# Kernel tuning notes

Measured on AMD Instinct MI355X. Metric: run time of the kernel, lower is better.

Reference implementation:

```python
import jax, jax.numpy as jnp
import numpy as np

SELECT_SIZE = 64
SM_SCALE = 0.07216878364870322  # 192 ** -0.5
V_HEAD_DIM = 128


def setup_inputs() -> dict:
    key = jax.random.key(0)
    k1, k2, k3, k4 = jax.random.split(key, 4)
    B, S, Hq, G, TOPK = 4, 2048, 16, 4, 16
    T = B * S
    NB = S // SELECT_SIZE  # 32 blocks per sequence
    q = jax.random.normal(k1, (T, Hq, 192), dtype=jnp.float32)
    k = jax.random.normal(k2, (T, Hq, 192), dtype=jnp.float32)
    v = jax.random.normal(k3, (T, Hq, V_HEAD_DIM), dtype=jnp.float32)
    idx = jax.random.randint(k4, (T, G, TOPK), 0, NB, dtype=jnp.int32)
    # guarantee block 0 is always selected so every causal row has >=1 valid key
    idx = idx.at[..., 0].set(0)
    idx = jnp.sort(idx, axis=-1)
    return {"q": q, "k": k, "v": v, "selected_indices": idx,
            "batch_size": B, "seq_len": S}


def reference(q, k, v, selected_indices, batch_size, seq_len):
    B, S = batch_size, seq_len
    Hq = q.shape[1]
    G = selected_indices.shape[1]
    Hg = Hq // G  # query heads per selection-score group
    nb = (S + SELECT_SIZE - 1) // SELECT_SIZE
    dv = v.shape[-1]

    # un-ragged: B equal-length sequences
    qg = q.reshape(B, S, G, Hg, -1)
    kg = k.reshape(B, S, G, Hg, -1)
    vg = v.reshape(B, S, G, Hg, -1)
    idx = selected_indices.reshape(B, S, G, -1)

    # which KV blocks are selected for each (query position, group): [B,S,G,nb]
    allowed_blk = (idx[..., None] == jnp.arange(nb, dtype=idx.dtype)).any(axis=-2)
    blk_of_pos = jnp.arange(S) // SELECT_SIZE
    pos_ok = allowed_blk[..., blk_of_pos]  # [B, Tq, G, Skv]
    causal = jnp.arange(S)[:, None] >= jnp.arange(S)[None, :]
    mask = pos_ok & causal[None, :, None, :]          # [B, Tq, G, Skv]
    mask = mask.transpose(0, 2, 1, 3)[:, :, None]      # [B, G, 1, Tq, Skv]

    scores = jnp.einsum('btghd,bsghd->bghts', qg, kg) * SM_SCALE
    scores = jnp.where(mask, scores, jnp.float32(-1e30))
    attn = jax.nn.softmax(scores, axis=-1)
    o = jnp.einsum('bghts,bsghd->btghd', attn, vg)
    return o.reshape(B * S, Hq * dv)
```

## Files before the change

kernel.cpp:

```cpp
#include <hip/hip_runtime.h>


typedef __attribute__((ext_vector_type(8))) _Float16 half8;
typedef __attribute__((ext_vector_type(4))) float f32x4;
typedef __attribute__((ext_vector_type(4))) unsigned int u32x4;

__device__ __forceinline__ half8 cvt8(const float4* p) {
  float4 a = p[0], b = p[1];
  half8 r;
  r[0] = (_Float16)a.x; r[1] = (_Float16)a.y; r[2] = (_Float16)a.z; r[3] = (_Float16)a.w;
  r[4] = (_Float16)b.x; r[5] = (_Float16)b.y; r[6] = (_Float16)b.z; r[7] = (_Float16)b.w;
  return r;
}

__device__ __forceinline__ half8 cvt8s(const float4* p, float s) {
  float4 a = p[0], b = p[1];
  half8 r;
  r[0] = (_Float16)(a.x * s); r[1] = (_Float16)(a.y * s);
  r[2] = (_Float16)(a.z * s); r[3] = (_Float16)(a.w * s);
  r[4] = (_Float16)(b.x * s); r[5] = (_Float16)(b.y * s);
  r[6] = (_Float16)(b.z * s); r[7] = (_Float16)(b.w * s);
  return r;
}

__device__ __forceinline__ void async16(const void* g, void* l) {
  __builtin_amdgcn_global_load_lds(
      (const __attribute__((address_space(1))) void*)g,
      (__attribute__((address_space(3))) void*)l, 16, 0, 0);
}

__device__ __forceinline__ f32x4 vmax4(f32x4 a, f32x4 b) {
  f32x4 r;
  r[0] = fmaxf(a[0], b[0]); r[1] = fmaxf(a[1], b[1]);
  r[2] = fmaxf(a[2], b[2]); r[3] = fmaxf(a[3], b[3]);
  return r;
}

__global__ __launch_bounds__(256) void kv_prep(const float* __restrict__ k,
                                               const float* __restrict__ v,
                                               _Float16* __restrict__ kf,
                                               _Float16* __restrict__ vf) {
  __shared__ float lb[64 * 196];
  int blk = blockIdx.x;
  int bh = blk >> 5, kb = blk & 31;
  int b = bh >> 4, h = bh & 15;
  int tid = threadIdx.x;

  const float* ksrc = k + ((long)(b * 2048 + kb * 64) * 16 + h) * 192;
#pragma unroll
  for (int it = 0; it < 12; ++it) {
    int idx = it * 256 + tid;
    int kk = idx / 48, c4 = idx - kk * 48;
    *(float4*)(&lb[kk * 196 + c4 * 4]) = *(const float4*)(ksrc + (long)kk * 3072 + c4 * 4);
  }
  __syncthreads();
  _Float16* kdst = kf + (long)blk * 12288;
#pragma unroll
  for (int it = 0; it < 6; ++it) {
    int oct = it * 256 + tid;
    int frag = oct >> 6, lane = oct & 63;
    int ntile = frag / 6, kc = frag - ntile * 6;
    int lm = lane & 15;
    int n = ((lm >> 2) << 4) + ntile * 4 + (lm & 3);
    int d = kc * 32 + ((lane >> 4) << 3);
    *(half8*)(kdst + (long)oct * 8) = cvt8((const float4*)(&lb[n * 196 + d]));
  }
  __syncthreads();

  const float* vsrc = v + ((long)(b * 2048 + kb * 64) * 16 + h) * 128;
#pragma unroll
  for (int it = 0; it < 8; ++it) {
    int idx = it * 256 + tid;
    int kk = idx >> 5, c4 = idx & 31;
    *(float4*)(&lb[kk * 132 + c4 * 4]) = *(const float4*)(vsrc + (long)kk * 2048 + c4 * 4);
  }
  __syncthreads();
  _Float16* vdst = vf + (long)blk * 8192;
#pragma unroll
  for (int it = 0; it < 4; ++it) {
    int oct = it * 256 + tid;
    int frag = oct >> 6, lane = oct & 63;
    int n0 = frag >> 1, kc = frag & 1;
    int dv = n0 * 16 + (lane & 15);
    int kbase = kc * 32 + ((lane >> 4) << 3);
    half8 o;
#pragma unroll
    for (int j = 0; j < 8; ++j) o[j] = (_Float16)lb[(kbase + j) * 132 + dv];
    *(half8*)(vdst + (long)oct * 8) = o;
  }
}

__global__ __launch_bounds__(256) void attn_main(const float* __restrict__ q,
                                                 const int* __restrict__ idx,
                                                 const _Float16* __restrict__ kf,
                                                 const _Float16* __restrict__ vf,
                                                 float* __restrict__ out) {
  constexpr float SCL = 0.07216878364870322f * 1.4426950408889634f;
  int id = (int)blockIdx.x;
  int qb = 31 - (id >> 6);
  int h = id & 15, b = (id >> 4) & 3, g = h >> 2;
  int tid = threadIdx.x;
  int w = tid >> 6, L = tid & 63;
  int Lm = L & 15, Lq = L >> 4;
  int m0 = w * 16;
  int t0 = b * 2048 + qb * 64;

  __shared__ __align__(16) char sh_k[24576];

  const char* kfb = (const char*)(kf + (long)((b * 16 + h) * 32) * 12288);
  const _Float16* vfb = vf + (long)((b * 16 + h) * 32) * 8192;

  auto stageK = [&](int kb) {
#pragma unroll
    for (int c = 0; c < 6; ++c) {
      int ch = w + c * 4;
      async16(kfb + (long)kb * 24576 + ch * 1024 + L * 16, sh_k + ch * 1024);
    }
  };

  half8 vr[16];
  auto loadV = [&](int kb) {
    const half8* vg = (const half8*)(vfb + (long)kb * 8192);
#pragma unroll
    for (int j = 0; j < 16; ++j) vr[j] = vg[j * 64 + L];
  };

  half8 qa[6];
  const float* qrow = q + ((long)(t0 + m0 + Lm) * 16 + h) * 192;
#pragma unroll
  for (int c = 0; c < 6; ++c) qa[c] = cvt8s((const float4*)(qrow + c * 32 + Lq * 8), SCL);

  unsigned rm = 0;
  {
    const int4* ip = (const int4*)(idx + ((long)(t0 + L) * 4 + g) * 16);
#pragma unroll
    for (int u = 0; u < 4; ++u) {
      int4 iv = ip[u];
      rm |= (1u << iv.x) | (1u << iv.y) | (1u << iv.z) | (1u << iv.w);
    }
  }
  unsigned bm = rm;
#pragma unroll
  for (int o = 1; o < 64; o <<= 1) bm |= __shfl_xor(bm, o, 64);
  unsigned mrow = __shfl(rm, m0 + Lm, 64);
  unsigned bmask = bm & ((2u << qb) - 1);

  stageK(0);
  loadV(0);

  f32x4 Oacc[8];
#pragma unroll
  for (int n0 = 0; n0 < 8; ++n0) Oacc[n0] = (f32x4){0.f, 0.f, 0.f, 0.f};
  float m_i = -1e30f, l_i = 0.f;

  unsigned rem = bmask;
  int kb = 0;

  for (;;) {
    rem &= rem - 1;
    int nxt = rem ? (int)__builtin_ctz(rem) : -1;

    asm volatile("s_waitcnt vmcnt(16)\n\ts_barrier" ::: "memory");

    const half8* lkf = (const half8*)sh_k;
    f32x4 S[4];
    __builtin_amdgcn_s_setprio(1);
#pragma unroll
    for (int nt = 0; nt < 4; ++nt) {
      f32x4 acc = {0.f, 0.f, 0.f, 0.f};
#pragma unroll
      for (int c = 0; c < 6; ++c)
        acc = __builtin_amdgcn_mfma_f32_16x16x32_f16(lkf[(nt * 6 + c) * 64 + L], qa[c], acc, 0, 0, 0);
      S[nt] = acc;
    }
    __builtin_amdgcn_s_setprio(0);

    asm volatile("s_waitcnt lgkmcnt(0)\n\ts_barrier" ::: "memory");
    if (nxt >= 0) stageK(nxt);

    float p[4][4];
    float msel = ((mrow >> kb) & 1u) ? 1.0f : 0.0f;
    if (kb != qb) {
      f32x4 t = vmax4(vmax4(S[0], S[1]), vmax4(S[2], S[3]));
      float rmax = fmaxf(fmaxf(t[0], t[1]), fmaxf(t[2], t[3]));
      rmax = fmaxf(rmax, __shfl_xor(rmax, 16));
      rmax = fmaxf(rmax, __shfl_xor(rmax, 32));
      if (__any(rmax > m_i)) {
        float mn = fmaxf(m_i, rmax);
        float av = __builtin_amdgcn_exp2f(m_i - mn);
        m_i = mn;
        l_i *= av;
#pragma unroll
        for (int n0 = 0; n0 < 8; ++n0) Oacc[n0] *= av;
      }
      float ps[4];
#pragma unroll
      for (int nt = 0; nt < 4; ++nt) {
        float s0 = 0.f, s1 = 0.f;
#pragma unroll
        for (int i = 0; i < 4; i += 2) {
          float a = __builtin_amdgcn_exp2f(S[nt][i] - m_i) * msel;
          float c = __builtin_amdgcn_exp2f(S[nt][i + 1] - m_i) * msel;
          p[nt][i] = a; p[nt][i + 1] = c;
          s0 += a; s1 += c;
        }
        ps[nt] = s0 + s1;
      }
      float psum = (ps[0] + ps[1]) + (ps[2] + ps[3]);
      psum += __shfl_xor(psum, 16);
      psum += __shfl_xor(psum, 32);
      l_i += psum;
    } else {
      float sc[4][4];
      float rmax = -1e30f;
#pragma unroll
      for (int nt = 0; nt < 4; ++nt)
#pragma unroll
        for (int i = 0; i < 4; ++i) {
          int key = Lq * 16 + nt * 4 + i;
          bool ok = (msel != 0.f) && (key <= m0 + Lm);
          float v = ok ? S[nt][i] : -1e30f;
          sc[nt][i] = v;
          rmax = fmaxf(rmax, v);
        }
      rmax = fmaxf(rmax, __shfl_xor(rmax, 16));
      rmax = fmaxf(rmax, __shfl_xor(rmax, 32));
      float mn = fmaxf(m_i, rmax);
      float av = __builtin_amdgcn_exp2f(m_i - mn);
      m_i = mn;
      float ps[4];
#pragma unroll
      for (int nt = 0; nt < 4; ++nt) {
        float s0 = 0.f;
#pragma unroll
        for (int i = 0; i < 4; ++i) {
          float a = __builtin_amdgcn_exp2f(sc[nt][i] - mn);
          p[nt][i] = a;
          s0 += a;
        }
        ps[nt] = s0;
      }
      float psum = (ps[0] + ps[1]) + (ps[2] + ps[3]);
      psum += __shfl_xor(psum, 16);
      psum += __shfl_xor(psum, 32);
      l_i = l_i * av + psum;
#pragma unroll
      for (int n0 = 0; n0 < 8; ++n0) Oacc[n0] *= av;
    }

    unsigned w8[8];
#pragma unroll
    for (int nt = 0; nt < 4; ++nt) {
      w8[2 * nt]     = __builtin_bit_cast(unsigned, __builtin_amdgcn_cvt_pkrtz(p[nt][0], p[nt][1]));
      w8[2 * nt + 1] = __builtin_bit_cast(unsigned, __builtin_amdgcn_cvt_pkrtz(p[nt][2], p[nt][3]));
    }
    half8 pfr[2];
#pragma unroll
    for (int kc = 0; kc < 2; ++kc) {
      int src = ((Lq >> 1) + 2 * kc) * 16 + Lm;
      u32x4 d;
#pragma unroll
      for (int u = 0; u < 4; ++u) {
        unsigned lo = (unsigned)__shfl((int)w8[u], src, 64);
        unsigned hi = (unsigned)__shfl((int)w8[u + 4], src, 64);
        d[u] = (Lq & 1) ? hi : lo;
      }
      pfr[kc] = __builtin_bit_cast(half8, d);
    }

    __builtin_amdgcn_s_setprio(1);
#pragma unroll
    for (int kc = 0; kc < 2; ++kc)
#pragma unroll
      for (int n0 = 0; n0 < 8; ++n0)
        Oacc[n0] = __builtin_amdgcn_mfma_f32_16x16x32_f16(vr[n0 * 2 + kc], pfr[kc], Oacc[n0], 0, 0, 0);
    __builtin_amdgcn_s_setprio(0);

    if (nxt < 0) break;
    loadV(nxt);
    kb = nxt;
  }

  float inv = 1.f / l_i;
  float* orow = out + (long)(t0 + m0 + Lm) * 2048 + h * 128 + Lq * 4;
#pragma unroll
  for (int n0 = 0; n0 < 8; ++n0) {
    f32x4 o = Oacc[n0] * inv;
    *(f32x4*)(orow + n0 * 16) = o;
  }
}

extern "C" void kernel_launch(void* const* d_in, const int* in_sizes, int n_in,
                              void* d_out, int out_size, void* d_ws, size_t ws_size,
                              hipStream_t stream) {
  const float* q = (const float*)d_in[0];
  const float* k = (const float*)d_in[1];
  const float* v = (const float*)d_in[2];
  const int* idx = (const int*)d_in[3];
  _Float16* kf = (_Float16*)d_ws;
  _Float16* vf = kf + (size_t)2048 * 12288;
  float* out = (float*)d_out;
  kv_prep<<<2048, 256, 0, stream>>>(k, v, kf, vf);
  attn_main<<<2048, 256, 0, stream>>>(q, idx, kf, vf, out);
}
```

Measured before the change: 443.1 us.

## Use two waves per block with 32 query rows each and stage V through LDS

```diff
diff --git a/kernel.cpp b/kernel.cpp
--- a/kernel.cpp
+++ b/kernel.cpp
@@ -90,7 +90,7 @@
   }
 }
 
-__global__ __launch_bounds__(256) void attn_main(const float* __restrict__ q,
+__global__ __launch_bounds__(128) void attn_main(const float* __restrict__ q,
                                                  const int* __restrict__ idx,
                                                  const _Float16* __restrict__ kf,
                                                  const _Float16* __restrict__ vf,
@@ -102,33 +102,45 @@
   int tid = threadIdx.x;
   int w = tid >> 6, L = tid & 63;
   int Lm = L & 15, Lq = L >> 4;
-  int m0 = w * 16;
+  int qoff = w * 32;
   int t0 = b * 2048 + qb * 64;
 
   __shared__ __align__(16) char sh_k[24576];
+  __shared__ __align__(16) char sh_v[16384];
 
   const char* kfb = (const char*)(kf + (long)((b * 16 + h) * 32) * 12288);
   const _Float16* vfb = vf + (long)((b * 16 + h) * 32) * 8192;
 
   auto stageK = [&](int kb) {
 #pragma unroll
-    for (int c = 0; c < 6; ++c) {
-      int ch = w + c * 4;
+    for (int c = 0; c < 12; ++c) {
+      int ch = w + c * 2;
       async16(kfb + (long)kb * 24576 + ch * 1024 + L * 16, sh_k + ch * 1024);
     }
   };
 
-  half8 vr[16];
-  auto loadV = [&](int kb) {
+  half8 vreg[8];
+  auto loadVreg = [&](int kb) {
     const half8* vg = (const half8*)(vfb + (long)kb * 8192);
 #pragma unroll
-    for (int j = 0; j < 16; ++j) vr[j] = vg[j * 64 + L];
+    for (int c = 0; c < 8; ++c) vreg[c] = vg[(w + c * 2) * 64 + L];
   };
-
-  half8 qa[6];
-  const float* qrow = q + ((long)(t0 + m0 + Lm) * 16 + h) * 192;
-#pragma unroll
-  for (int c = 0; c < 6; ++c) qa[c] = cvt8s((const float4*)(qrow + c * 32 + Lq * 8), SCL);
+  auto writeV = [&]() {
+#pragma unroll
+    for (int c = 0; c < 8; ++c)
+      *(half8*)(sh_v + (w + c * 2) * 1024 + L * 16) = vreg[c];
+  };
+
+  stageK(0);
+  loadVreg(0);
+
+  half8 qa[2][6];
+#pragma unroll
+  for (int j = 0; j < 2; ++j) {
+    const float* qrow = q + ((long)(t0 + qoff + j * 16 + Lm) * 16 + h) * 192;
+#pragma unroll
+    for (int c = 0; c < 6; ++c) qa[j][c] = cvt8s((const float4*)(qrow + c * 32 + Lq * 8), SCL);
+  }
 
   unsigned rm = 0;
   {
@@ -142,16 +154,21 @@
   unsigned bm = rm;
 #pragma unroll
   for (int o = 1; o < 64; o <<= 1) bm |= __shfl_xor(bm, o, 64);
-  unsigned mrow = __shfl(rm, m0 + Lm, 64);
+  unsigned mrow[2];
+#pragma unroll
+  for (int j = 0; j < 2; ++j) mrow[j] = __shfl(rm, qoff + j * 16 + Lm, 64);
   unsigned bmask = bm & ((2u << qb) - 1);
 
-  stageK(0);
-  loadV(0);
-
-  f32x4 Oacc[8];
-#pragma unroll
-  for (int n0 = 0; n0 < 8; ++n0) Oacc[n0] = (f32x4){0.f, 0.f, 0.f, 0.f};
-  float m_i = -1e30f, l_i = 0.f;
+  asm volatile("s_waitcnt vmcnt(0)" ::: "memory");
+  writeV();
+  asm volatile("s_waitcnt lgkmcnt(0)\n\ts_barrier" ::: "memory");
+
+  f32x4 Oacc[2][8];
+#pragma unroll
+  for (int j = 0; j < 2; ++j)
+#pragma unroll
+    for (int n0 = 0; n0 < 8; ++n0) Oacc[j][n0] = (f32x4){0.f, 0.f, 0.f, 0.f};
+  float m_i[2] = {-1e30f, -1e30f}, l_i[2] = {0.f, 0.f};
 
   unsigned rem = bmask;
   int kb = 0;
@@ -160,133 +177,150 @@
     rem &= rem - 1;
     int nxt = rem ? (int)__builtin_ctz(rem) : -1;
 
-    asm volatile("s_waitcnt vmcnt(16)\n\ts_barrier" ::: "memory");
-
     const half8* lkf = (const half8*)sh_k;
-    f32x4 S[4];
+    f32x4 S[2][4];
+#pragma unroll
+    for (int j = 0; j < 2; ++j)
+#pragma unroll
+      for (int nt = 0; nt < 4; ++nt) S[j][nt] = (f32x4){0.f, 0.f, 0.f, 0.f};
     __builtin_amdgcn_s_setprio(1);
 #pragma unroll
-    for (int nt = 0; nt < 4; ++nt) {
-      f32x4 acc = {0.f, 0.f, 0.f, 0.f};
-#pragma unroll
-      for (int c = 0; c < 6; ++c)
-        acc = __builtin_amdgcn_mfma_f32_16x16x32_f16(lkf[(nt * 6 + c) * 64 + L], qa[c], acc, 0, 0, 0);
-      S[nt] = acc;
-    }
+    for (int nt = 0; nt < 4; ++nt)
+#pragma unroll
+      for (int c = 0; c < 6; ++c) {
+        half8 ka = lkf[(nt * 6 + c) * 64 + L];
+        S[0][nt] = __builtin_amdgcn_mfma_f32_16x16x32_f16(ka, qa[0][c], S[0][nt], 0, 0, 0);
+        S[1][nt] = __builtin_amdgcn_mfma_f32_16x16x32_f16(ka, qa[1][c], S[1][nt], 0, 0, 0);
+      }
     __builtin_amdgcn_s_setprio(0);
 
     asm volatile("s_waitcnt lgkmcnt(0)\n\ts_barrier" ::: "memory");
-    if (nxt >= 0) stageK(nxt);
-
-    float p[4][4];
-    float msel = ((mrow >> kb) & 1u) ? 1.0f : 0.0f;
-    if (kb != qb) {
-      f32x4 t = vmax4(vmax4(S[0], S[1]), vmax4(S[2], S[3]));
-      float rmax = fmaxf(fmaxf(t[0], t[1]), fmaxf(t[2], t[3]));
-      rmax = fmaxf(rmax, __shfl_xor(rmax, 16));
-      rmax = fmaxf(rmax, __shfl_xor(rmax, 32));
-      if (__any(rmax > m_i)) {
-        float mn = fmaxf(m_i, rmax);
-        float av = __builtin_amdgcn_exp2f(m_i - mn);
-        m_i = mn;
-        l_i *= av;
-#pragma unroll
-        for (int n0 = 0; n0 < 8; ++n0) Oacc[n0] *= av;
-      }
-      float ps[4];
+    if (nxt >= 0) {
+      stageK(nxt);
+      loadVreg(nxt);
+    }
+
+    half8 pfr[2][2];
+#pragma unroll
+    for (int j = 0; j < 2; ++j) {
+      float p[4][4];
+      float msel = ((mrow[j] >> kb) & 1u) ? 1.0f : 0.0f;
+      if (kb != qb) {
+        f32x4 t = vmax4(vmax4(S[j][0], S[j][1]), vmax4(S[j][2], S[j][3]));
+        float rmax = fmaxf(fmaxf(t[0], t[1]), fmaxf(t[2], t[3]));
+        rmax = fmaxf(rmax, __shfl_xor(rmax, 16));
+        rmax = fmaxf(rmax, __shfl_xor(rmax, 32));
+        if (__any(rmax > m_i[j])) {
+          float mn = fmaxf(m_i[j], rmax);
+          float av = __builtin_amdgcn_exp2f(m_i[j] - mn);
+          m_i[j] = mn;
+          l_i[j] *= av;
+#pragma unroll
+          for (int n0 = 0; n0 < 8; ++n0) Oacc[j][n0] *= av;
+        }
+        float ps[4];
+#pragma unroll
+        for (int nt = 0; nt < 4; ++nt) {
+          float s0 = 0.f, s1 = 0.f;
+#pragma unroll
+          for (int i = 0; i < 4; i += 2) {
+            float a = __builtin_amdgcn_exp2f(S[j][nt][i] - m_i[j]) * msel;
+            float c = __builtin_amdgcn_exp2f(S[j][nt][i + 1] - m_i[j]) * msel;
+            p[nt][i] = a; p[nt][i + 1] = c;
+            s0 += a; s1 += c;
+          }
+          ps[nt] = s0 + s1;
+        }
+        float psum = (ps[0] + ps[1]) + (ps[2] + ps[3]);
+        psum += __shfl_xor(psum, 16);
+        psum += __shfl_xor(psum, 32);
+        l_i[j] += psum;
+      } else {
+        int qrow = qoff + j * 16 + Lm;
+        float sc[4][4];
+        float rmax = -1e30f;
+#pragma unroll
+        for (int nt = 0; nt < 4; ++nt)
+#pragma unroll
+          for (int i = 0; i < 4; ++i) {
+            int key = Lq * 16 + nt * 4 + i;
+            bool ok = (msel != 0.f) && (key <= qrow);
+            float v = ok ? S[j][nt][i] : -1e30f;
+            sc[nt][i] = v;
+            rmax = fmaxf(rmax, v);
+          }
+        rmax = fmaxf(rmax, __shfl_xor(rmax, 16));
+        rmax = fmaxf(rmax, __shfl_xor(rmax, 32));
+        float mn = fmaxf(m_i[j], rmax);
+        float av = __builtin_amdgcn_exp2f(m_i[j] - mn);
+        m_i[j] = mn;
+        float ps[4];
+#pragma unroll
+        for (int nt = 0; nt < 4; ++nt) {
+          float s0 = 0.f;
+#pragma unroll
+          for (int i = 0; i < 4; ++i) {
+            float a = __builtin_amdgcn_exp2f(sc[nt][i] - mn);
+            p[nt][i] = a;
+            s0 += a;
+          }
+          ps[nt] = s0;
+        }
+        float psum = (ps[0] + ps[1]) + (ps[2] + ps[3]);
+        psum += __shfl_xor(psum, 16);
+        psum += __shfl_xor(psum, 32);
+        l_i[j] = l_i[j] * av + psum;
+#pragma unroll
+        for (int n0 = 0; n0 < 8; ++n0) Oacc[j][n0] *= av;
+      }
+
+      unsigned w8[8];
 #pragma unroll
       for (int nt = 0; nt < 4; ++nt) {
-        float s0 = 0.f, s1 = 0.f;
-#pragma unroll
-        for (int i = 0; i < 4; i += 2) {
-          float a = __builtin_amdgcn_exp2f(S[nt][i] - m_i) * msel;
-          float c = __builtin_amdgcn_exp2f(S[nt][i + 1] - m_i) * msel;
-          p[nt][i] = a; p[nt][i + 1] = c;
-          s0 += a; s1 += c;
+        w8[2 * nt]     = __builtin_bit_cast(unsigned, __builtin_amdgcn_cvt_pkrtz(p[nt][0], p[nt][1]));
+        w8[2 * nt + 1] = __builtin_bit_cast(unsigned, __builtin_amdgcn_cvt_pkrtz(p[nt][2], p[nt][3]));
+      }
+#pragma unroll
+      for (int kc = 0; kc < 2; ++kc) {
+        int src = ((Lq >> 1) + 2 * kc) * 16 + Lm;
+        u32x4 d;
+#pragma unroll
+        for (int u = 0; u < 4; ++u) {
+          unsigned lo = (unsigned)__shfl((int)w8[u], src, 64);
+          unsigned hi = (unsigned)__shfl((int)w8[u + 4], src, 64);
+          d[u] = (Lq & 1) ? hi : lo;
         }
-        ps[nt] = s0 + s1;
-      }
-      float psum = (ps[0] + ps[1]) + (ps[2] + ps[3]);
-      psum += __shfl_xor(psum, 16);
-      psum += __shfl_xor(psum, 32);
-      l_i += psum;
-    } else {
-      float sc[4][4];
-      float rmax = -1e30f;
-#pragma unroll
-      for (int nt = 0; nt < 4; ++nt)
-#pragma unroll
-        for (int i = 0; i < 4; ++i) {
-          int key = Lq * 16 + nt * 4 + i;
-          bool ok = (msel != 0.f) && (key <= m0 + Lm);
-          float v = ok ? S[nt][i] : -1e30f;
-          sc[nt][i] = v;
-          rmax = fmaxf(rmax, v);
-        }
-      rmax = fmaxf(rmax, __shfl_xor(rmax, 16));
-      rmax = fmaxf(rmax, __shfl_xor(rmax, 32));
-      float mn = fmaxf(m_i, rmax);
-      float av = __builtin_amdgcn_exp2f(m_i - mn);
-      m_i = mn;
-      float ps[4];
-#pragma unroll
-      for (int nt = 0; nt < 4; ++nt) {
-        float s0 = 0.f;
-#pragma unroll
-        for (int i = 0; i < 4; ++i) {
-          float a = __builtin_amdgcn_exp2f(sc[nt][i] - mn);
-          p[nt][i] = a;
-          s0 += a;
-        }
-        ps[nt] = s0;
-      }
-      float psum = (ps[0] + ps[1]) + (ps[2] + ps[3]);
-      psum += __shfl_xor(psum, 16);
-      psum += __shfl_xor(psum, 32);
-      l_i = l_i * av + psum;
-#pragma unroll
-      for (int n0 = 0; n0 < 8; ++n0) Oacc[n0] *= av;
-    }
-
-    unsigned w8[8];
-#pragma unroll
-    for (int nt = 0; nt < 4; ++nt) {
-      w8[2 * nt]     = __builtin_bit_cast(unsigned, __builtin_amdgcn_cvt_pkrtz(p[nt][0], p[nt][1]));
-      w8[2 * nt + 1] = __builtin_bit_cast(unsigned, __builtin_amdgcn_cvt_pkrtz(p[nt][2], p[nt][3]));
-    }
-    half8 pfr[2];
-#pragma unroll
-    for (int kc = 0; kc < 2; ++kc) {
-      int src = ((Lq >> 1) + 2 * kc) * 16 + Lm;
-      u32x4 d;
-#pragma unroll
-      for (int u = 0; u < 4; ++u) {
-        unsigned lo = (unsigned)__shfl((int)w8[u], src, 64);
-        unsigned hi = (unsigned)__shfl((int)w8[u + 4], src, 64);
-        d[u] = (Lq & 1) ? hi : lo;
-      }
-      pfr[kc] = __builtin_bit_cast(half8, d);
-    }
-
+        pfr[j][kc] = __builtin_bit_cast(half8, d);
+      }
+    }
+
+    const half8* lvf = (const half8*)sh_v;
     __builtin_amdgcn_s_setprio(1);
 #pragma unroll
     for (int kc = 0; kc < 2; ++kc)
 #pragma unroll
-      for (int n0 = 0; n0 < 8; ++n0)
-        Oacc[n0] = __builtin_amdgcn_mfma_f32_16x16x32_f16(vr[n0 * 2 + kc], pfr[kc], Oacc[n0], 0, 0, 0);
+      for (int n0 = 0; n0 < 8; ++n0) {
+        half8 va = lvf[(n0 * 2 + kc) * 64 + L];
+        Oacc[0][n0] = __builtin_amdgcn_mfma_f32_16x16x32_f16(va, pfr[0][kc], Oacc[0][n0], 0, 0, 0);
+        Oacc[1][n0] = __builtin_amdgcn_mfma_f32_16x16x32_f16(va, pfr[1][kc], Oacc[1][n0], 0, 0, 0);
+      }
     __builtin_amdgcn_s_setprio(0);
 
     if (nxt < 0) break;
-    loadV(nxt);
+    asm volatile("s_waitcnt lgkmcnt(0)\n\ts_waitcnt vmcnt(0)\n\ts_barrier" ::: "memory");
+    writeV();
     kb = nxt;
   }
 
-  float inv = 1.f / l_i;
-  float* orow = out + (long)(t0 + m0 + Lm) * 2048 + h * 128 + Lq * 4;
-#pragma unroll
-  for (int n0 = 0; n0 < 8; ++n0) {
-    f32x4 o = Oacc[n0] * inv;
-    *(f32x4*)(orow + n0 * 16) = o;
+#pragma unroll
+  for (int j = 0; j < 2; ++j) {
+    float inv = 1.f / l_i[j];
+    float* orow = out + (long)(t0 + qoff + j * 16 + Lm) * 2048 + h * 128 + Lq * 4;
+#pragma unroll
+    for (int n0 = 0; n0 < 8; ++n0) {
+      f32x4 o = Oacc[j][n0] * inv;
+      *(f32x4*)(orow + n0 * 16) = o;
+    }
   }
 }
 
@@ -301,5 +335,5 @@
   _Float16* vf = kf + (size_t)2048 * 12288;
   float* out = (float*)d_out;
   kv_prep<<<2048, 256, 0, stream>>>(k, v, kf, vf);
-  attn_main<<<2048, 256, 0, stream>>>(q, idx, kf, vf, out);
-}
+  attn_main<<<2048, 128, 0, stream>>>(q, idx, kf, vf, out);
+}
```

Result: slower. 481.9 us (+8.8%).
